# Performance work log

Hardware: AMD Instinct MI355X
Metric: run time of the kernel (lower is better)

Reference implementation:

```python
import jax, jax.numpy as jnp
import numpy as np

D_MODEL, D_STATE, EXPAND = 1024, 32, 2
D_INNER = D_MODEL * EXPAND
B, L = 2, 2048


def setup_inputs() -> dict:
    key = jax.random.key(0)
    ks = jax.random.split(key, 10)
    s = 0.02
    return {
        "x": jax.random.normal(ks[0], (B, L, D_MODEL), dtype=jnp.float32),
        "W_in": jax.random.normal(ks[1], (D_INNER * 2, D_MODEL), dtype=jnp.float32) * s,
        "conv_w": jax.random.normal(ks[2], (D_INNER, 1, 3), dtype=jnp.float32) * 0.3,
        "conv_b": jax.random.normal(ks[3], (D_INNER,), dtype=jnp.float32) * 0.01,
        "A_log": jax.random.normal(ks[4], (D_INNER, D_STATE), dtype=jnp.float32),
        "D_skip": jnp.ones((D_INNER,), dtype=jnp.float32),
        "W_xproj": jax.random.normal(ks[5], (D_STATE * 2 + 1, D_INNER), dtype=jnp.float32) * s,
        "W_dt": jax.random.normal(ks[6], (D_INNER, 1), dtype=jnp.float32) * s,
        "b_dt": jax.random.normal(ks[7], (D_INNER,), dtype=jnp.float32) * 0.01,
        "alpha": jnp.asarray(0.5, dtype=jnp.float32),
        "W_out": jax.random.normal(ks[8], (D_MODEL, D_INNER), dtype=jnp.float32) * s,
    }


def _silu(v):
    return v * jax.nn.sigmoid(v)


def _forward(x, W_in, conv_w, conv_b, A_log, D_skip, W_xproj, W_dt, b_dt, alpha, W_out):
    # in_proj: (B, L, 2*d_inner) -> split into x_in, z
    xz = x @ W_in.T
    x_in, z = jnp.split(xz, 2, axis=-1)

    # depthwise conv1d, kernel 3, padding 1 (same-length, non-causal, as in source)
    xc = jax.lax.conv_general_dilated(
        x_in.transpose(0, 2, 1), conv_w, window_strides=(1,), padding=[(1, 1)],
        dimension_numbers=("NCH", "OIH", "NCH"), feature_group_count=D_INNER,
    ) + conv_b[None, :, None]
    x_conv = _silu(xc.transpose(0, 2, 1))  # (B, L, d_inner)

    # x_proj -> dt_raw (1), B_ssm (N), C_ssm (N)
    proj = x_conv @ W_xproj.T
    dt_raw = proj[..., :1]
    B_ssm = proj[..., 1:1 + D_STATE]
    C_ssm = proj[..., 1 + D_STATE:]
    dt = jax.nn.softplus(dt_raw @ W_dt.T + b_dt)  # (B, L, d_inner)

    A_real = -jnp.exp(A_log)           # (d_inner, d_state)
    a = jax.nn.sigmoid(alpha)

    def step(h, inp):
        dt_t, B_t, C_t, u_t = inp      # (B,d_inner), (B,N), (B,N), (B,d_inner)
        dtA = A_real[None] * dt_t[:, :, None]               # (B, d_inner, N)
        A_d = a * jnp.exp(dtA) + (1.0 - a) / (1.0 - 0.5 * dtA + 1e-6)
        h = A_d * h + (dt_t * u_t)[:, :, None] * B_t[:, None, :]
        y_t = jnp.einsum("bn,bdn->bd", C_t, h) + D_skip * u_t
        return h, y_t

    h0 = jnp.zeros((x.shape[0], D_INNER, D_STATE), dtype=x.dtype)
    xs = (dt.transpose(1, 0, 2), B_ssm.transpose(1, 0, 2),
          C_ssm.transpose(1, 0, 2), x_conv.transpose(1, 0, 2))
    _, ys = jax.lax.scan(step, h0, xs)   # (L, B, d_inner)
    y = ys.transpose(1, 0, 2) * _silu(z)
    return y @ W_out.T


def reference(x, W_in, conv_w, conv_b, A_log, D_skip, W_xproj, W_dt, b_dt, alpha, W_out):
    return _forward(x, W_in, conv_w, conv_b, A_log, D_skip, W_xproj, W_dt, b_dt, alpha, W_out)
```

## Files before the change

kernel.cpp:

```cpp
#include <hip/hip_runtime.h>

#define DM   1024
#define DI   2048
#define DST  32
#define NB   2
#define LSEQ 2048
#define BL   (NB*LSEQ)
#define LC   32
#define NC   64

using bf16   = __bf16;
using bf16x4 = __attribute__((ext_vector_type(4))) __bf16;
using bf16x8 = __attribute__((ext_vector_type(8))) __bf16;
using f32x4  = __attribute__((ext_vector_type(4))) float;
using f16x2  = __attribute__((ext_vector_type(2))) _Float16;

#define AS1(p) ((const __attribute__((address_space(1))) void*)(p))
#define AS3(p) ((__attribute__((address_space(3))) void*)(p))

static __device__ __forceinline__ float sigmoidf_(float x) {
  return 1.f / (1.f + __expf(-x));
}

static __device__ __forceinline__ f16x2 pack_f16x2(float a, float b) {
  return __builtin_bit_cast(f16x2, __builtin_amdgcn_cvt_pkrtz(a, b));
}

static __device__ __forceinline__ float exp2_(float x) {
#if __has_builtin(__builtin_amdgcn_exp2f)
  return __builtin_amdgcn_exp2f(x);
#else
  return exp2f(x);
#endif
}

__global__ __launch_bounds__(256) void cast_bf16_kernel(
    const float* __restrict__ in, bf16* __restrict__ out, int n4) {
  int i = blockIdx.x * 256 + threadIdx.x;
  if (i >= n4) return;
  f32x4 v = ((const f32x4*)in)[i];
  bf16x4 o;
  #pragma unroll
  for (int j = 0; j < 4; ++j) o[j] = (bf16)v[j];
  ((bf16x4*)out)[i] = o;
}

__global__ __launch_bounds__(256) void padcast_wxp_kernel(
    const float* __restrict__ in, bf16* __restrict__ out) {
  int i = blockIdx.x * 256 + threadIdx.x;
  int k4 = i & 511;
  int r  = i >> 9;
  int src = (r < 64) ? (r + 1) : ((r == 127) ? 0 : -1);
  f32x4 v = {0.f, 0.f, 0.f, 0.f};
  if (src >= 0) v = *(const f32x4*)(in + (size_t)src * 2048 + k4 * 4);
  bf16x4 o;
  #pragma unroll
  for (int j = 0; j < 4; ++j) o[j] = (bf16)v[j];
  ((bf16x4*)out)[i] = o;
}

__global__ __launch_bounds__(256) void gemm_lds(
    const bf16* __restrict__ A, const bf16* __restrict__ B,
    float* __restrict__ C, int M, int N, int K, int nz) {
  __shared__ bf16 As2[4][128][8];
  __shared__ bf16 Bs2[4][128][8];

  int tid  = threadIdx.x;
  int bm   = blockIdx.y, bn = blockIdx.x;
  int row0 = bm * 128, col0 = bn * 128;
  int w    = tid >> 6, lane = tid & 63;
  int wr   = w >> 1, wc = w & 1;
  int lr   = lane & 15, lk = lane >> 4;

  int seg = K / nz;
  int kb  = blockIdx.z * seg, ke = kb + seg;
  float* Cz = C + (size_t)blockIdx.z * ((size_t)M * N);

  f32x4 acc[4][4];
  #pragma unroll
  for (int i = 0; i < 4; ++i)
    #pragma unroll
    for (int j = 0; j < 4; ++j) acc[i][j] = f32x4{0.f, 0.f, 0.f, 0.f};

  int j0 = w * 64 + lane, j1 = 256 + w * 64 + lane;
  int ks0 = j0 >> 7, r0s = j0 & 127;
  int ks1 = j1 >> 7, r1s = j1 & 127;
  const bf16* Ag0 = A + (size_t)(row0 + r0s) * K + ks0 * 8;
  const bf16* Ag1 = A + (size_t)(row0 + r1s) * K + ks1 * 8;
  const bf16* Bg0 = B + (size_t)(col0 + r0s) * K + ks0 * 8;
  const bf16* Bg1 = B + (size_t)(col0 + r1s) * K + ks1 * 8;
  bf16* AsL = &As2[0][0][0];
  bf16* BsL = &Bs2[0][0][0];
  int base0 = (w * 64) * 8;
  int base1 = (256 + w * 64) * 8;

  for (int k0 = kb; k0 < ke; k0 += 32) {
    __builtin_amdgcn_global_load_lds(AS1(Ag0 + k0), AS3(AsL + base0), 16, 0, 0);
    __builtin_amdgcn_global_load_lds(AS1(Ag1 + k0), AS3(AsL + base1), 16, 0, 0);
    __builtin_amdgcn_global_load_lds(AS1(Bg0 + k0), AS3(BsL + base0), 16, 0, 0);
    __builtin_amdgcn_global_load_lds(AS1(Bg1 + k0), AS3(BsL + base1), 16, 0, 0);
    __syncthreads();

    bf16x8 af[4], bff[4];
    #pragma unroll
    for (int mi = 0; mi < 4; ++mi)
      af[mi] = *(const bf16x8*)&As2[lk][wr * 64 + mi * 16 + lr][0];
    #pragma unroll
    for (int ni = 0; ni < 4; ++ni)
      bff[ni] = *(const bf16x8*)&Bs2[lk][wc * 64 + ni * 16 + lr][0];

    #pragma unroll
    for (int mi = 0; mi < 4; ++mi)
      #pragma unroll
      for (int ni = 0; ni < 4; ++ni)
        acc[mi][ni] = __builtin_amdgcn_mfma_f32_16x16x32_bf16(
            af[mi], bff[ni], acc[mi][ni], 0, 0, 0);
    __syncthreads();
  }

  #pragma unroll
  for (int mi = 0; mi < 4; ++mi)
    #pragma unroll
    for (int ni = 0; ni < 4; ++ni) {
      int r0 = row0 + wr * 64 + mi * 16 + lk * 4;
      int c  = col0 + wc * 64 + ni * 16 + lr;
      #pragma unroll
      for (int r = 0; r < 4; ++r)
        Cz[(size_t)(r0 + r) * N + c] = acc[mi][ni][r];
    }
}

__global__ __launch_bounds__(256) void reduce_proj_kernel(
    const float* __restrict__ part, float* __restrict__ proj) {
  int i = blockIdx.x * 256 + threadIdx.x;
  f32x4 s = ((const f32x4*)part)[i];
  #pragma unroll
  for (int z = 1; z < 8; ++z) s += ((const f32x4*)part)[(size_t)z * 131072 + i];
  ((f32x4*)proj)[i] = s;
}

__global__ __launch_bounds__(256) void conv_silu_kernel(
    const float* __restrict__ xz, bf16* __restrict__ xconv,
    const float* __restrict__ conv_w, const float* __restrict__ conv_b) {
  int i = blockIdx.x * 256 + threadIdx.x;
  int d4 = i & 511;
  int d  = d4 * 4;
  int bl = i >> 9;
  int l  = bl & (LSEQ - 1);

  const float* base = xz + (size_t)bl * (2 * DI) + d;
  f32x4 zero = {0.f, 0.f, 0.f, 0.f};
  f32x4 xm = (l > 0)        ? *(const f32x4*)(base - 2 * DI) : zero;
  f32x4 xc = *(const f32x4*)(base);
  f32x4 xp = (l < LSEQ - 1) ? *(const f32x4*)(base + 2 * DI) : zero;

  bf16x4 o;
  #pragma unroll
  for (int j = 0; j < 4; ++j) {
    float w0 = conv_w[(d + j) * 3 + 0];
    float w1 = conv_w[(d + j) * 3 + 1];
    float w2 = conv_w[(d + j) * 3 + 2];
    float v = fmaf(w0, xm[j], fmaf(w1, xc[j], fmaf(w2, xp[j], conv_b[d + j])));
    v = v * sigmoidf_(v);
    o[j] = (bf16)v;
  }
  *(bf16x4*)(xconv + (size_t)bl * DI + d) = o;
}

__global__ __launch_bounds__(256) void dtprep_kernel(
    const float* __restrict__ proj, const bf16* __restrict__ xconv,
    const float* __restrict__ W_dt, const float* __restrict__ b_dt,
    unsigned int* __restrict__ dtp) {
  int i = blockIdx.x * 256 + threadIdx.x;
  int d4 = (i & 511) * 4;
  int bl = i >> 9;
  float dtraw = proj[(size_t)bl * 128 + 127];
  f32x4 wd = *(const f32x4*)(W_dt + d4);
  f32x4 bd = *(const f32x4*)(b_dt + d4);
  bf16x4 uu = *(const bf16x4*)(xconv + (size_t)bl * DI + d4);
  uint4 o;
  #pragma unroll
  for (int j = 0; j < 4; ++j) {
    float s  = fmaf(dtraw, wd[j], bd[j]);
    float dt = (s > 15.f) ? s : __logf(1.f + __expf(s));
    float dtu = dt * (float)uu[j];
    f16x2 pk = pack_f16x2(dt, dtu);
    ((unsigned int*)&o)[j] = __builtin_bit_cast(unsigned int, pk);
  }
  *(uint4*)(dtp + (size_t)bl * 4096 + d4) = o;
}


__global__ __launch_bounds__(256, 4) void scan_phase1(
    const float* __restrict__ proj, const unsigned int* __restrict__ dtp,
    const float* __restrict__ A_log, const float* __restrict__ alpha,
    unsigned int* __restrict__ PH) {
  int wid = threadIdx.x >> 6, lane = threadIdx.x & 63;
  int d = blockIdx.x * 256 + wid * 64 + lane;
  int b = blockIdx.y, c = blockIdx.z;

  float aG = sigmoidf_(alpha[0]), omA = 1.f - aG;

  float Ar2[DST];
  #pragma unroll
  for (int n = 0; n < DST; n += 4) {
    f32x4 al = *(const f32x4*)(A_log + (size_t)d * DST + n);
    #pragma unroll
    for (int j = 0; j < 4; ++j) Ar2[n + j] = -__expf(al[j]) * 1.44269504f;
  }

  const float* pb = proj + ((size_t)b * LSEQ + c * LC) * 128;
  const unsigned int* dc = dtp + ((size_t)b * LSEQ + c * LC) * 4096 + d;

  float h[DST], P[DST];
  #pragma unroll
  for (int n = 0; n < DST; ++n) { h[n] = 0.f; P[n] = 1.f; }

  #pragma unroll 2
  for (int t = 0; t < LC; ++t) {
    f16x2 dw = __builtin_bit_cast(f16x2, dc[(size_t)t * 4096]);
    float dt = (float)dw[0], dtu = (float)dw[1];
    const float* pr = pb + (size_t)t * 128;
    #pragma unroll
    for (int n4 = 0; n4 < 8; ++n4) {
      f32x4 Bq = *(const f32x4*)(pr + n4 * 4);
      #pragma unroll
      for (int j = 0; j < 4; ++j) {
        int n = n4 * 4 + j;
        float t1  = dt * Ar2[n];
        float ex  = exp2_(t1);
        float den = fmaf(t1, -0.34657359f, 1.000001f);
        float Ad  = fmaf(aG, ex, omA * __builtin_amdgcn_rcpf(den));
        P[n] *= Ad;
        h[n] = fmaf(Ad, h[n], dtu * Bq[j]);
      }
    }
  }
  size_t ob = (((size_t)c * NB + b) * DI + d) * DST;
  #pragma unroll
  for (int n4 = 0; n4 < 8; ++n4) {
    uint4 o;
    #pragma unroll
    for (int j = 0; j < 4; ++j) {
      int n = n4 * 4 + j;
      ((unsigned int*)&o)[j] =
          __builtin_bit_cast(unsigned int, pack_f16x2(P[n], h[n]));
    }
    *(uint4*)(PH + ob + n4 * 4) = o;
  }
}

__global__ __launch_bounds__(256) void scan_phase2(unsigned int* __restrict__ PH) {
  int i = blockIdx.x * 256 + threadIdx.x;
  float H = 0.f;
  #pragma unroll 4
  for (int c = 0; c < NC; ++c) {
    size_t idx = (size_t)c * (NB * DI * DST) + i;
    f16x2 ph = __builtin_bit_cast(f16x2, PH[idx]);
    ((float*)PH)[idx] = H;
    H = fmaf((float)ph[0], H, (float)ph[1]);
  }
}

__global__ __launch_bounds__(256, 4) void scan_phase3(
    const float* __restrict__ proj, const unsigned int* __restrict__ dtp,
    const float* __restrict__ xzf,
    const bf16* __restrict__ xconv,
    const float* __restrict__ A_log, const float* __restrict__ D_skip,
    const float* __restrict__ alpha, const float* __restrict__ PH,
    bf16* __restrict__ yb) {
  int wid = threadIdx.x >> 6, lane = threadIdx.x & 63;
  int d = blockIdx.x * 256 + wid * 64 + lane;
  int b = blockIdx.y, c = blockIdx.z;

  float aG = sigmoidf_(alpha[0]), omA = 1.f - aG;
  float Dsk = D_skip[d];

  float Ar2[DST];
  #pragma unroll
  for (int n = 0; n < DST; n += 4) {
    f32x4 al = *(const f32x4*)(A_log + (size_t)d * DST + n);
    #pragma unroll
    for (int j = 0; j < 4; ++j) Ar2[n + j] = -__expf(al[j]) * 1.44269504f;
  }

  float h[DST];
  size_t ob = (((size_t)c * NB + b) * DI + d) * DST;
  #pragma unroll
  for (int n = 0; n < DST; n += 4) {
    f32x4 hv = *(const f32x4*)(PH + ob + n);
    #pragma unroll
    for (int j = 0; j < 4; ++j) h[n + j] = hv[j];
  }

  const float* pb = proj + ((size_t)b * LSEQ + c * LC) * 128;
  const unsigned int* dc = dtp + ((size_t)b * LSEQ + c * LC) * 4096 + d;
  const bf16*  uc = xconv + ((size_t)b * LSEQ + c * LC) * DI + d;
  const float* zc = xzf + ((size_t)b * LSEQ + c * LC) * 4096 + 2048 + d;
  bf16*        yc = yb  + ((size_t)b * LSEQ + c * LC) * DI + d;

  #pragma unroll 2
  for (int t = 0; t < LC; ++t) {
    f16x2 dw = __builtin_bit_cast(f16x2, dc[(size_t)t * 4096]);
    float dt = (float)dw[0], dtu = (float)dw[1];
    const float* pr = pb + (size_t)t * 128;
    float p0 = 0.f, p1 = 0.f, p2 = 0.f, p3 = 0.f;
    #pragma unroll
    for (int n4 = 0; n4 < 8; ++n4) {
      f32x4 Bq = *(const f32x4*)(pr + n4 * 4);
      f32x4 Cq = *(const f32x4*)(pr + 32 + n4 * 4);
      #pragma unroll
      for (int j = 0; j < 4; ++j) {
        int n = n4 * 4 + j;
        float t1  = dt * Ar2[n];
        float ex  = exp2_(t1);
        float den = fmaf(t1, -0.34657359f, 1.000001f);
        float Ad  = fmaf(aG, ex, omA * __builtin_amdgcn_rcpf(den));
        h[n] = fmaf(Ad, h[n], dtu * Bq[j]);
        if (j == 0)      p0 = fmaf(Cq[j], h[n], p0);
        else if (j == 1) p1 = fmaf(Cq[j], h[n], p1);
        else if (j == 2) p2 = fmaf(Cq[j], h[n], p2);
        else             p3 = fmaf(Cq[j], h[n], p3);
      }
    }
    float part = (p0 + p1) + (p2 + p3);
    float u = (float)uc[(size_t)t * DI];
    float z = zc[(size_t)t * 4096];
    float y = fmaf(Dsk, u, part);
    y *= z * sigmoidf_(z);
    yc[(size_t)t * DI] = (bf16)y;
  }
}

extern "C" void kernel_launch(void* const* d_in, const int* in_sizes, int n_in,
                              void* d_out, int out_size, void* d_ws, size_t ws_size,
                              hipStream_t stream) {
  const float* x      = (const float*)d_in[0];
  const float* W_in   = (const float*)d_in[1];
  const float* conv_w = (const float*)d_in[2];
  const float* conv_b = (const float*)d_in[3];
  const float* A_log  = (const float*)d_in[4];
  const float* D_skip = (const float*)d_in[5];
  const float* W_xprj = (const float*)d_in[6];
  const float* W_dt   = (const float*)d_in[7];
  const float* b_dt   = (const float*)d_in[8];
  const float* alpha  = (const float*)d_in[9];
  const float* W_out  = (const float*)d_in[10];

  char* ws = (char*)d_ws;
  float* xz    = (float*)(ws + 0);
  bf16*  xconv = (bf16*) (ws + 67108864);
  float* proj  = (float*)(ws + 83886080);
  bf16*  woutb = (bf16*) (ws + 85983232);
  bf16*  wxpb  = (bf16*) (ws + 90177536);
  bf16*  yb    = (bf16*) (ws + 90701824);
  unsigned int* PH = (unsigned int*)(ws + 107479040);
  bf16*  xb    = (bf16*) (ws + 107479040);
  bf16*  winb  = (bf16*) (ws + 115867648);
  float* projp = (float*)(ws + 107479040);
  unsigned int* dtp = (unsigned int*)xz;

  float* out = (float*)d_out;

  cast_bf16_kernel<<<4096, 256, 0, stream>>>(x, xb, BL * DM / 4);
  cast_bf16_kernel<<<4096, 256, 0, stream>>>(W_in, winb, 2 * DI * DM / 4);
  cast_bf16_kernel<<<2048, 256, 0, stream>>>(W_out, woutb, DM * DI / 4);
  padcast_wxp_kernel<<<256, 256, 0, stream>>>(W_xprj, wxpb);

  gemm_lds<<<dim3(32, 32, 1), 256, 0, stream>>>(xb, winb, xz, BL, 2 * DI, DM, 1);

  conv_silu_kernel<<<8192, 256, 0, stream>>>(xz, xconv, conv_w, conv_b);

  gemm_lds<<<dim3(1, 32, 8), 256, 0, stream>>>(xconv, wxpb, projp, BL, 128, DI, 8);
  reduce_proj_kernel<<<512, 256, 0, stream>>>(projp, proj);

  dtprep_kernel<<<8192, 256, 0, stream>>>(proj, xconv, W_dt, b_dt, dtp);

  scan_phase1<<<dim3(DI / 256, NB, NC), 256, 0, stream>>>(proj, dtp, A_log,
                                                          alpha, PH);
  scan_phase2<<<512, 256, 0, stream>>>(PH);
  scan_phase3<<<dim3(DI / 256, NB, NC), 256, 0, stream>>>(proj, dtp, xz, xconv,
                                                          A_log, D_skip, alpha,
                                                          (const float*)PH, yb);

  gemm_lds<<<dim3(8, 32, 1), 256, 0, stream>>>(yb, woutb, out, BL, DM, DI, 1);
}
```

Measured before the change: 406.3 us.

## Split SSM state dimension across two half-waves in scan phases

Each channel's 32-element state is now split across two lanes, each holding 16 states, so every wave covers 32 channels instead of 64 and the grid doubles. Phase 3 combines the two partial C·h sums with a cross-lane xor shuffle, and only the lower half-wave writes the gated output. The aim is to roughly halve per-thread register use so launch bounds can allow 8 blocks per CU and raise occupancy for the latency-bound scan. In exchange, the dt/u/z loads are duplicated across half-waves, a shuffle is added per timestep, and the output store uses only half the lanes.

```diff
diff --git a/kernel.cpp b/kernel.cpp
--- a/kernel.cpp
+++ b/kernel.cpp
@@ -191,30 +191,32 @@
 }
 
 
-__global__ __launch_bounds__(256, 4) void scan_phase1(
+__global__ __launch_bounds__(256, 8) void scan_phase1(
     const float* __restrict__ proj, const unsigned int* __restrict__ dtp,
     const float* __restrict__ A_log, const float* __restrict__ alpha,
     unsigned int* __restrict__ PH) {
   int wid = threadIdx.x >> 6, lane = threadIdx.x & 63;
-  int d = blockIdx.x * 256 + wid * 64 + lane;
+  int dl = lane & 31, nh = lane >> 5;
+  int d = blockIdx.x * 128 + wid * 32 + dl;
   int b = blockIdx.y, c = blockIdx.z;
+  int n0 = nh * 16;
 
   float aG = sigmoidf_(alpha[0]), omA = 1.f - aG;
 
-  float Ar2[DST];
-  #pragma unroll
-  for (int n = 0; n < DST; n += 4) {
-    f32x4 al = *(const f32x4*)(A_log + (size_t)d * DST + n);
+  float Ar2[16];
+  #pragma unroll
+  for (int n = 0; n < 16; n += 4) {
+    f32x4 al = *(const f32x4*)(A_log + (size_t)d * DST + n0 + n);
     #pragma unroll
     for (int j = 0; j < 4; ++j) Ar2[n + j] = -__expf(al[j]) * 1.44269504f;
   }
 
-  const float* pb = proj + ((size_t)b * LSEQ + c * LC) * 128;
+  const float* pb = proj + ((size_t)b * LSEQ + c * LC) * 128 + n0;
   const unsigned int* dc = dtp + ((size_t)b * LSEQ + c * LC) * 4096 + d;
 
-  float h[DST], P[DST];
-  #pragma unroll
-  for (int n = 0; n < DST; ++n) { h[n] = 0.f; P[n] = 1.f; }
+  float h[16], P[16];
+  #pragma unroll
+  for (int n = 0; n < 16; ++n) { h[n] = 0.f; P[n] = 1.f; }
 
   #pragma unroll 2
   for (int t = 0; t < LC; ++t) {
@@ -222,7 +224,7 @@
     float dt = (float)dw[0], dtu = (float)dw[1];
     const float* pr = pb + (size_t)t * 128;
     #pragma unroll
-    for (int n4 = 0; n4 < 8; ++n4) {
+    for (int n4 = 0; n4 < 4; ++n4) {
       f32x4 Bq = *(const f32x4*)(pr + n4 * 4);
       #pragma unroll
       for (int j = 0; j < 4; ++j) {
@@ -236,9 +238,9 @@
       }
     }
   }
-  size_t ob = (((size_t)c * NB + b) * DI + d) * DST;
-  #pragma unroll
-  for (int n4 = 0; n4 < 8; ++n4) {
+  size_t ob = (((size_t)c * NB + b) * DI + d) * DST + n0;
+  #pragma unroll
+  for (int n4 = 0; n4 < 4; ++n4) {
     uint4 o;
     #pragma unroll
     for (int j = 0; j < 4; ++j) {
@@ -262,7 +264,7 @@
   }
 }
 
-__global__ __launch_bounds__(256, 4) void scan_phase3(
+__global__ __launch_bounds__(256, 8) void scan_phase3(
     const float* __restrict__ proj, const unsigned int* __restrict__ dtp,
     const float* __restrict__ xzf,
     const bf16* __restrict__ xconv,
@@ -270,30 +272,32 @@
     const float* __restrict__ alpha, const float* __restrict__ PH,
     bf16* __restrict__ yb) {
   int wid = threadIdx.x >> 6, lane = threadIdx.x & 63;
-  int d = blockIdx.x * 256 + wid * 64 + lane;
+  int dl = lane & 31, nh = lane >> 5;
+  int d = blockIdx.x * 128 + wid * 32 + dl;
   int b = blockIdx.y, c = blockIdx.z;
+  int n0 = nh * 16;
 
   float aG = sigmoidf_(alpha[0]), omA = 1.f - aG;
   float Dsk = D_skip[d];
 
-  float Ar2[DST];
-  #pragma unroll
-  for (int n = 0; n < DST; n += 4) {
-    f32x4 al = *(const f32x4*)(A_log + (size_t)d * DST + n);
+  float Ar2[16];
+  #pragma unroll
+  for (int n = 0; n < 16; n += 4) {
+    f32x4 al = *(const f32x4*)(A_log + (size_t)d * DST + n0 + n);
     #pragma unroll
     for (int j = 0; j < 4; ++j) Ar2[n + j] = -__expf(al[j]) * 1.44269504f;
   }
 
-  float h[DST];
-  size_t ob = (((size_t)c * NB + b) * DI + d) * DST;
-  #pragma unroll
-  for (int n = 0; n < DST; n += 4) {
+  float h[16];
+  size_t ob = (((size_t)c * NB + b) * DI + d) * DST + n0;
+  #pragma unroll
+  for (int n = 0; n < 16; n += 4) {
     f32x4 hv = *(const f32x4*)(PH + ob + n);
     #pragma unroll
     for (int j = 0; j < 4; ++j) h[n + j] = hv[j];
   }
 
-  const float* pb = proj + ((size_t)b * LSEQ + c * LC) * 128;
+  const float* pb = proj + ((size_t)b * LSEQ + c * LC) * 128 + n0;
   const unsigned int* dc = dtp + ((size_t)b * LSEQ + c * LC) * 4096 + d;
   const bf16*  uc = xconv + ((size_t)b * LSEQ + c * LC) * DI + d;
   const float* zc = xzf + ((size_t)b * LSEQ + c * LC) * 4096 + 2048 + d;
@@ -306,7 +310,7 @@
     const float* pr = pb + (size_t)t * 128;
     float p0 = 0.f, p1 = 0.f, p2 = 0.f, p3 = 0.f;
     #pragma unroll
-    for (int n4 = 0; n4 < 8; ++n4) {
+    for (int n4 = 0; n4 < 4; ++n4) {
       f32x4 Bq = *(const f32x4*)(pr + n4 * 4);
       f32x4 Cq = *(const f32x4*)(pr + 32 + n4 * 4);
       #pragma unroll
@@ -324,11 +328,14 @@
       }
     }
     float part = (p0 + p1) + (p2 + p3);
-    float u = (float)uc[(size_t)t * DI];
-    float z = zc[(size_t)t * 4096];
-    float y = fmaf(Dsk, u, part);
-    y *= z * sigmoidf_(z);
-    yc[(size_t)t * DI] = (bf16)y;
+    part += __shfl_xor(part, 32);
+    if (nh == 0) {
+      float u = (float)uc[(size_t)t * DI];
+      float z = zc[(size_t)t * 4096];
+      float y = fmaf(Dsk, u, part);
+      y *= z * sigmoidf_(z);
+      yc[(size_t)t * DI] = (bf16)y;
+    }
   }
 }
 
@@ -376,10 +383,10 @@
 
   dtprep_kernel<<<8192, 256, 0, stream>>>(proj, xconv, W_dt, b_dt, dtp);
 
-  scan_phase1<<<dim3(DI / 256, NB, NC), 256, 0, stream>>>(proj, dtp, A_log,
+  scan_phase1<<<dim3(DI / 128, NB, NC), 256, 0, stream>>>(proj, dtp, A_log,
                                                           alpha, PH);
   scan_phase2<<<512, 256, 0, stream>>>(PH);
-  scan_phase3<<<dim3(DI / 256, NB, NC), 256, 0, stream>>>(proj, dtp, xz, xconv,
+  scan_phase3<<<dim3(DI / 128, NB, NC), 256, 0, stream>>>(proj, dtp, xz, xconv,
                                                           A_log, D_skip, alpha,
                                                           (const float*)PH, yb);
 
```

After: 591.5 us. 45.6% more time.
